# Kernel tuning notes

Measured on AMD Instinct MI355X. Metric: run time of the kernel, lower is better.

Reference implementation:

```python
import jax, jax.numpy as jnp
import numpy as np

BN_EPS = 1e-5


def spmm(rows, cols, vals, x):
    # Sparse [V,V] @ x for x: [B, V, F]. COO (rows, cols, vals) with E nnz.
    B, V, F = x.shape
    xt = jnp.transpose(x, (1, 0, 2)).reshape(V, B * F)      # [V, B*F]
    msg = xt[cols] * vals[:, None]                           # [E, B*F]
    y = jax.ops.segment_sum(msg, rows, num_segments=V)       # [V, B*F]
    return jnp.transpose(y.reshape(V, B, F), (1, 0, 2))      # [B, V, F]


def cheb_conv(rows, cols, vals, x, W, b):
    # Chebyshev graph conv: out = sum_k T_k(L) x @ W[k] + b ; W: [K, Fin, Fout]
    K = W.shape[0]
    x0 = x
    out = jnp.einsum('bvi,io->bvo', x0, W[0])
    if K > 1:
        x1 = spmm(rows, cols, vals, x0)
        out = out + jnp.einsum('bvi,io->bvo', x1, W[1])
        for k in range(2, K):
            x2 = 2.0 * spmm(rows, cols, vals, x1) - x0
            out = out + jnp.einsum('bvi,io->bvo', x2, W[k])
            x0, x1 = x1, x2
    return out + b


def bn_relu(x, gamma, beta):
    # BatchNorm1d (training stats) over (batch, nodes) per channel, then ReLU.
    m = jnp.mean(x, axis=(0, 1))
    v = jnp.var(x, axis=(0, 1))
    y = (x - m) * jax.lax.rsqrt(v + BN_EPS) * gamma + beta
    return jax.nn.relu(y)


def setup_inputs() -> dict:
    key = jax.random.key(0)
    ks = jax.random.split(key, 8)
    V, DEG, B, CIN, COUT = 49152, 20, 2, 128, 64
    x = jax.random.normal(ks[0], (B, V, CIN), dtype=jnp.float32)
    # HEALPix-like sparse Laplacian: diagonal + 20 random neighbors per node
    self_idx = jnp.arange(V, dtype=jnp.int32)
    nbr = jax.random.randint(ks[1], (V * DEG,), 0, V, dtype=jnp.int32)
    rows = jnp.concatenate([self_idx, jnp.repeat(self_idx, DEG)])
    cols = jnp.concatenate([self_idx, nbr])
    vals = jax.random.normal(ks[2], (V * (DEG + 1),), dtype=jnp.float32) * 0.1
    def w(k, shape):
        fan_in = shape[0] * shape[1]
        return jax.random.normal(k, shape, dtype=jnp.float32) * np.float32(np.sqrt(2.0 / fan_in))
    return {
        'x': x, 'rows': rows, 'cols': cols, 'vals': vals,
        'W1': w(ks[3], (1, CIN, COUT)), 'b1': jnp.zeros((COUT,), jnp.float32),
        'g1': jnp.ones((COUT,), jnp.float32), 'be1': jnp.zeros((COUT,), jnp.float32),
        'W2': w(ks[4], (3, COUT, COUT)), 'b2': jnp.zeros((COUT,), jnp.float32),
        'g2': jnp.ones((COUT,), jnp.float32), 'be2': jnp.zeros((COUT,), jnp.float32),
        'W3': w(ks[5], (1, COUT, CIN)), 'b3': jnp.zeros((CIN,), jnp.float32),
        'g3': jnp.ones((CIN,), jnp.float32), 'be3': jnp.zeros((CIN,), jnp.float32),
    }


def reference(x, rows, cols, vals, W1, b1, g1, be1, W2, b2, g2, be2, W3, b3, g3, be3):
    h = bn_relu(cheb_conv(rows, cols, vals, x, W1, b1), g1, be1)   # [B,V,64]
    h = bn_relu(cheb_conv(rows, cols, vals, h, W2, b2), g2, be2)   # [B,V,64]
    h = bn_relu(cheb_conv(rows, cols, vals, h, W3, b3), g3, be3)   # [B,V,128]
    return h
```

## Files before the change

kernel.cpp:

```cpp
#include <hip/hip_runtime.h>

#define VN 49152
#define DEG 20
#define NB 2
#define MROWS (NB * VN)

static constexpr float BN_EPS = 1e-5f;

typedef short bf16x8 __attribute__((ext_vector_type(8)));
typedef float floatx4 __attribute__((ext_vector_type(4)));

__device__ __forceinline__ unsigned short f2bf(float f) {
  unsigned int u = __builtin_bit_cast(unsigned int, f);
  u += 0x7FFFu + ((u >> 16) & 1u);
  return (unsigned short)(u >> 16);
}
__device__ __forceinline__ float bf2f(unsigned short h) {
  unsigned int u = ((unsigned int)h) << 16;
  return __builtin_bit_cast(float, u);
}
__device__ __forceinline__ float bflo(unsigned int u) {
  return __builtin_bit_cast(float, u << 16);
}
__device__ __forceinline__ float bfhi(unsigned int u) {
  return __builtin_bit_cast(float, u & 0xFFFF0000u);
}
__device__ __forceinline__ unsigned int packbf(float a, float b) {
  return (unsigned int)f2bf(a) | ((unsigned int)f2bf(b) << 16);
}
__device__ __forceinline__ void bfunpack8(const uint4& d, float* f) {
  f[0] = bflo(d.x); f[1] = bfhi(d.x); f[2] = bflo(d.y); f[3] = bfhi(d.y);
  f[4] = bflo(d.z); f[5] = bfhi(d.z); f[6] = bflo(d.w); f[7] = bfhi(d.w);
}


#define LDA1 136
__global__ __launch_bounds__(256) void gemm1(const float* __restrict__ X,
    const float* __restrict__ W, const float* __restrict__ bias,
    unsigned short* __restrict__ Y, float* __restrict__ st) {
  __shared__ unsigned short As[128 * LDA1];
  __shared__ unsigned short Bs[64 * LDA1];
  __shared__ float sred[128];
  int t = threadIdx.x;
  int row0 = blockIdx.x * 128;
  if (t < 128) sred[t] = 0.f;
  const float* Xt = X + (size_t)row0 * 128;
  #pragma unroll
  for (int c = 0; c < 16; ++c) {
    int f4i = c * 256 + t;
    int row = f4i >> 5, k = (f4i & 31) * 4;
    float4 v = *(const float4*)(Xt + row * 128 + k);
    *(uint2*)(&As[row * LDA1 + k]) = make_uint2(packbf(v.x, v.y), packbf(v.z, v.w));
  }
  #pragma unroll
  for (int c = 0; c < 32; ++c) {
    int f = c * 256 + t;
    int k = f >> 6, n = f & 63;
    Bs[n * LDA1 + k] = f2bf(W[f]);
  }
  __syncthreads();
  int l = t & 63, wv = t >> 6;
  int lr = l & 15, q = l >> 4;
  int m0 = wv * 32;
  floatx4 acc[2][4];
  #pragma unroll
  for (int mi = 0; mi < 2; ++mi)
    #pragma unroll
    for (int ni = 0; ni < 4; ++ni) acc[mi][ni] = (floatx4)(0.f);
  #pragma unroll
  for (int ks = 0; ks < 128; ks += 32) {
    bf16x8 af[2], bfr[4];
    #pragma unroll
    for (int mi = 0; mi < 2; ++mi)
      af[mi] = *(const bf16x8*)(&As[(m0 + mi * 16 + lr) * LDA1 + ks + q * 8]);
    #pragma unroll
    for (int ni = 0; ni < 4; ++ni)
      bfr[ni] = *(const bf16x8*)(&Bs[(ni * 16 + lr) * LDA1 + ks + q * 8]);
    #pragma unroll
    for (int mi = 0; mi < 2; ++mi)
      #pragma unroll
      for (int ni = 0; ni < 4; ++ni)
        acc[mi][ni] = __builtin_amdgcn_mfma_f32_16x16x32_bf16(af[mi], bfr[ni], acc[mi][ni], 0, 0, 0);
  }
  int b = (row0 >= VN) ? 1 : 0;
  int vbase = row0 - b * VN + m0;
  #pragma unroll
  for (int ni = 0; ni < 4; ++ni) {
    int col = ni * 16 + lr;
    float bv = bias[col];
    size_t sub = (size_t)(b * 2 + (col >> 5)) * VN;
    float s = 0.f, s2 = 0.f;
    #pragma unroll
    for (int mi = 0; mi < 2; ++mi)
      #pragma unroll
      for (int r = 0; r < 4; ++r) {
        float y = acc[mi][ni][r] + bv;
        s += y; s2 += y * y;
        int v = vbase + mi * 16 + q * 4 + r;
        Y[(sub + v) * 32 + (col & 31)] = f2bf(y);
      }
    atomicAdd(&sred[col], s);
    atomicAdd(&sred[64 + col], s2);
  }
  __syncthreads();
  if (t < 128) atomicAdd(&st[t], sred[t]);
}

__global__ __launch_bounds__(256) void spmm1(const unsigned short* __restrict__ T1,
    const int* __restrict__ cols, const float* __restrict__ vals,
    const float* __restrict__ st1, const float* __restrict__ g1,
    const float* __restrict__ be1, unsigned short* __restrict__ X1out) {
  __shared__ float scS[64], shS[64];
  int t = threadIdx.x;
  if (t < 64) {
    float mean = st1[t] * (1.f / MROWS);
    float var = st1[64 + t] * (1.f / MROWS) - mean * mean;
    float sc = g1[t] * rsqrtf(var + BN_EPS);
    scS[t] = sc; shS[t] = be1[t] - mean * sc;
  }
  __syncthreads();
  int g = blockIdx.x;
  int combo = (g & 7) >> 1;
  int rg = ((g >> 3) << 1) | (g & 1);
  int wv = t >> 6, lane = t & 63;
  int v = rg * 64 + wv * 16 + (lane >> 2);
  int ch0 = (lane & 3) * 8;
  int chg = (combo & 1) * 32 + ch0;
  float sc8[8], sh8[8];
  #pragma unroll
  for (int j = 0; j < 8; ++j) { sc8[j] = scS[chg + j]; sh8[j] = shS[chg + j]; }
  const unsigned short* __restrict__ plane = T1 + (size_t)combo * VN * 32;
  int4  c4[5];
  float4 w4[5];
  const int4*   __restrict__ cp4 = (const int4*)(cols + VN + v * DEG);
  const float4* __restrict__ vp4 = (const float4*)(vals + VN + v * DEG);
  #pragma unroll
  for (int j = 0; j < 5; ++j) { c4[j] = cp4[j]; w4[j] = vp4[j]; }
  float a[8];
  {
    float w0 = vals[v];
    uint4 d = *(const uint4*)(plane + (size_t)v * 32 + ch0);
    float f[8]; bfunpack8(d, f);
    #pragma unroll
    for (int j = 0; j < 8; ++j) {
      float h = fmaf(f[j], sc8[j], sh8[j]); h = h > 0.f ? h : 0.f;
      a[j] = w0 * h;
    }
  }
  #pragma unroll
  for (int jj = 0; jj < 5; ++jj) {
    const int cj[4] = {c4[jj].x, c4[jj].y, c4[jj].z, c4[jj].w};
    const float wj[4] = {w4[jj].x, w4[jj].y, w4[jj].z, w4[jj].w};
    #pragma unroll
    for (int e = 0; e < 4; ++e) {
      uint4 d = *(const uint4*)(plane + (size_t)cj[e] * 32 + ch0);
      float f[8]; bfunpack8(d, f);
      float w = wj[e];
      #pragma unroll
      for (int j = 0; j < 8; ++j) {
        float h = fmaf(f[j], sc8[j], sh8[j]); h = h > 0.f ? h : 0.f;
        a[j] = fmaf(h, w, a[j]);
      }
    }
  }
  uint4 o;
  o.x = packbf(a[0], a[1]); o.y = packbf(a[2], a[3]);
  o.z = packbf(a[4], a[5]); o.w = packbf(a[6], a[7]);
  *(uint4*)(X1out + (size_t)combo * VN * 32 + (size_t)v * 32 + ch0) = o;
}

__global__ __launch_bounds__(256) void spmm2(const unsigned short* __restrict__ X1,
    const unsigned short* __restrict__ T1, const int* __restrict__ cols,
    const float* __restrict__ vals, const float* __restrict__ st1,
    const float* __restrict__ g1, const float* __restrict__ be1,
    unsigned short* __restrict__ X2out) {
  __shared__ float scS[64], shS[64];
  int t = threadIdx.x;
  if (t < 64) {
    float mean = st1[t] * (1.f / MROWS);
    float var = st1[64 + t] * (1.f / MROWS) - mean * mean;
    float sc = g1[t] * rsqrtf(var + BN_EPS);
    scS[t] = sc; shS[t] = be1[t] - mean * sc;
  }
  __syncthreads();
  int g = blockIdx.x;
  int combo = (g & 7) >> 1;
  int rg = ((g >> 3) << 1) | (g & 1);
  int wv = t >> 6, lane = t & 63;
  int v = rg * 64 + wv * 16 + (lane >> 2);
  int ch0 = (lane & 3) * 8;
  int chg = (combo & 1) * 32 + ch0;
  const size_t pbase = (size_t)combo * VN * 32;
  const size_t myoff = pbase + (size_t)v * 32 + ch0;
  const unsigned short* __restrict__ plane = X1 + pbase;
  int4  c4[5];
  float4 w4[5];
  const int4*   __restrict__ cp4 = (const int4*)(cols + VN + v * DEG);
  const float4* __restrict__ vp4 = (const float4*)(vals + VN + v * DEG);
  #pragma unroll
  for (int j = 0; j < 5; ++j) { c4[j] = cp4[j]; w4[j] = vp4[j]; }
  float a[8];
  {
    float w0 = vals[v];
    uint4 d = *(const uint4*)(X1 + myoff);
    float f[8]; bfunpack8(d, f);
    #pragma unroll
    for (int j = 0; j < 8; ++j) a[j] = w0 * f[j];
  }
  #pragma unroll
  for (int jj = 0; jj < 5; ++jj) {
    const int cj[4] = {c4[jj].x, c4[jj].y, c4[jj].z, c4[jj].w};
    const float wj[4] = {w4[jj].x, w4[jj].y, w4[jj].z, w4[jj].w};
    #pragma unroll
    for (int e = 0; e < 4; ++e) {
      uint4 d = *(const uint4*)(plane + (size_t)cj[e] * 32 + ch0);
      float f[8]; bfunpack8(d, f);
      float w = wj[e];
      #pragma unroll
      for (int j = 0; j < 8; ++j) a[j] = fmaf(f[j], w, a[j]);
    }
  }
  uint4 tv = *(const uint4*)(T1 + myoff);
  float f[8]; bfunpack8(tv, f);
  float h[8];
  #pragma unroll
  for (int j = 0; j < 8; ++j) {
    float y = fmaf(f[j], scS[chg + j], shS[chg + j]);
    h[j] = y > 0.f ? y : 0.f;
  }
  uint4 o;
  o.x = packbf(2.f * a[0] - h[0], 2.f * a[1] - h[1]);
  o.y = packbf(2.f * a[2] - h[2], 2.f * a[3] - h[3]);
  o.z = packbf(2.f * a[4] - h[4], 2.f * a[5] - h[5]);
  o.w = packbf(2.f * a[6] - h[6], 2.f * a[7] - h[7]);
  *(uint4*)(X2out + myoff) = o;
}

#define LDA2 72
__global__ __launch_bounds__(256) void gemm2(const unsigned short* __restrict__ T1,
    const unsigned short* __restrict__ X1, const unsigned short* __restrict__ X2,
    const float* __restrict__ st1, const float* __restrict__ g1,
    const float* __restrict__ be1, const float* __restrict__ W,
    const float* __restrict__ bias, unsigned short* __restrict__ Y,
    float* __restrict__ st2) {
  __shared__ unsigned short As[128 * LDA2];
  __shared__ unsigned short Bs[64 * LDA2];
  __shared__ float sred[128];
  __shared__ float scS[64], shS[64];
  int t = threadIdx.x;
  int row0 = blockIdx.x * 128;
  int b = (row0 >= VN) ? 1 : 0;
  int b2 = b * 2;
  int vb0 = row0 - b * VN;
  if (t < 128) sred[t] = 0.f;
  if (t < 64) {
    float mean = st1[t] * (1.f / MROWS);
    float var = st1[64 + t] * (1.f / MROWS) - mean * mean;
    float sc = g1[t] * rsqrtf(var + BN_EPS);
    scS[t] = sc; shS[t] = be1[t] - mean * sc;
  }
  __syncthreads();
  int l = t & 63, wv = t >> 6;
  int lr = l & 15, q = l >> 4;
  int m0 = wv * 32;
  floatx4 acc[2][4];
  #pragma unroll
  for (int mi = 0; mi < 2; ++mi)
    #pragma unroll
    for (int ni = 0; ni < 4; ++ni) acc[mi][ni] = (floatx4)(0.f);

  auto stage_b = [&](const float* Wt) {
    #pragma unroll
    for (int c = 0; c < 16; ++c) {
      int f = c * 256 + t;
      int k = f >> 6, n = f & 63;
      Bs[n * LDA2 + k] = f2bf(Wt[f]);
    }
  };
  auto mfma_tile = [&]() {
    #pragma unroll
    for (int ks = 0; ks < 64; ks += 32) {
      bf16x8 af[2], bfr[4];
      #pragma unroll
      for (int mi = 0; mi < 2; ++mi)
        af[mi] = *(const bf16x8*)(&As[(m0 + mi * 16 + lr) * LDA2 + ks + q * 8]);
      #pragma unroll
      for (int ni = 0; ni < 4; ++ni)
        bfr[ni] = *(const bf16x8*)(&Bs[(ni * 16 + lr) * LDA2 + ks + q * 8]);
      #pragma unroll
      for (int mi = 0; mi < 2; ++mi)
        #pragma unroll
        for (int ni = 0; ni < 4; ++ni)
          acc[mi][ni] = __builtin_amdgcn_mfma_f32_16x16x32_bf16(af[mi], bfr[ni], acc[mi][ni], 0, 0, 0);
    }
  };

  #pragma unroll
  for (int c8 = 0; c8 < 8; ++c8) {
    int i = c8 * 256 + t;
    int row = i >> 4, k = (i & 15) * 4;
    const unsigned short* src = T1 + ((size_t)(b2 + (k >> 5)) * VN + vb0 + row) * 32 + (k & 31);
    uint2 rawv = *(const uint2*)src;
    float y0 = fmaf(bflo(rawv.x), scS[k + 0], shS[k + 0]);
    float y1 = fmaf(bfhi(rawv.x), scS[k + 1], shS[k + 1]);
    float y2 = fmaf(bflo(rawv.y), scS[k + 2], shS[k + 2]);
    float y3 = fmaf(bfhi(rawv.y), scS[k + 3], shS[k + 3]);
    y0 = y0 > 0.f ? y0 : 0.f; y1 = y1 > 0.f ? y1 : 0.f;
    y2 = y2 > 0.f ? y2 : 0.f; y3 = y3 > 0.f ? y3 : 0.f;
    *(uint2*)(&As[row * LDA2 + k]) = make_uint2(packbf(y0, y1), packbf(y2, y3));
  }
  stage_b(W);
  __syncthreads();
  mfma_tile();
  __syncthreads();

  #pragma unroll
  for (int c8 = 0; c8 < 8; ++c8) {
    int i = c8 * 256 + t;
    int row = i >> 4, k = (i & 15) * 4;
    const unsigned short* src = X1 + ((size_t)(b2 + (k >> 5)) * VN + vb0 + row) * 32 + (k & 31);
    *(uint2*)(&As[row * LDA2 + k]) = *(const uint2*)src;
  }
  stage_b(W + 64 * 64);
  __syncthreads();
  mfma_tile();
  __syncthreads();

  #pragma unroll
  for (int c8 = 0; c8 < 8; ++c8) {
    int i = c8 * 256 + t;
    int row = i >> 4, k = (i & 15) * 4;
    const unsigned short* src = X2 + ((size_t)(b2 + (k >> 5)) * VN + vb0 + row) * 32 + (k & 31);
    *(uint2*)(&As[row * LDA2 + k]) = *(const uint2*)src;
  }
  stage_b(W + 2 * 64 * 64);
  __syncthreads();
  mfma_tile();

  int vbase = vb0 + m0;
  #pragma unroll
  for (int ni = 0; ni < 4; ++ni) {
    int col = ni * 16 + lr;
    float bv = bias[col];
    size_t sub = (size_t)(b2 + (col >> 5)) * VN;
    float s = 0.f, s2 = 0.f;
    #pragma unroll
    for (int mi = 0; mi < 2; ++mi)
      #pragma unroll
      for (int r = 0; r < 4; ++r) {
        float y = acc[mi][ni][r] + bv;
        s += y; s2 += y * y;
        int v = vbase + mi * 16 + q * 4 + r;
        Y[(sub + v) * 32 + (col & 31)] = f2bf(y);
      }
    atomicAdd(&sred[col], s);
    atomicAdd(&sred[64 + col], s2);
  }
  __syncthreads();
  if (t < 128) atomicAdd(&st2[t], sred[t]);
}

#define LDC3 136
__global__ __launch_bounds__(256) void gemm3(const unsigned short* __restrict__ X,
    const float* __restrict__ W, const float* __restrict__ bias,
    const float* __restrict__ st2, const float* __restrict__ gamma,
    const float* __restrict__ beta, unsigned short* __restrict__ Y,
    float* __restrict__ st3) {
  __shared__ unsigned short smem[18432];
  __shared__ float sred[256];
  __shared__ float scS[64], shS[64];
  unsigned short* As = smem;
  unsigned short* Bs = smem + 128 * LDA2;
  int t = threadIdx.x;
  int row0 = blockIdx.x * 128;
  int b = (row0 >= VN) ? 1 : 0;
  int b2 = b * 2;
  int vb0 = row0 - b * VN;
  sred[t] = 0.f;
  if (t < 64) {
    float mean = st2[t] * (1.f / MROWS);
    float var = st2[64 + t] * (1.f / MROWS) - mean * mean;
    float sc = gamma[t] * rsqrtf(var + BN_EPS);
    scS[t] = sc; shS[t] = beta[t] - mean * sc;
  }
  __syncthreads();
  #pragma unroll
  for (int c8 = 0; c8 < 8; ++c8) {
    int i = c8 * 256 + t;
    int row = i >> 4, k = (i & 15) * 4;
    const unsigned short* src = X + ((size_t)(b2 + (k >> 5)) * VN + vb0 + row) * 32 + (k & 31);
    uint2 rawv = *(const uint2*)src;
    float y0 = fmaf(bflo(rawv.x), scS[k + 0], shS[k + 0]);
    float y1 = fmaf(bfhi(rawv.x), scS[k + 1], shS[k + 1]);
    float y2 = fmaf(bflo(rawv.y), scS[k + 2], shS[k + 2]);
    float y3 = fmaf(bfhi(rawv.y), scS[k + 3], shS[k + 3]);
    y0 = y0 > 0.f ? y0 : 0.f; y1 = y1 > 0.f ? y1 : 0.f;
    y2 = y2 > 0.f ? y2 : 0.f; y3 = y3 > 0.f ? y3 : 0.f;
    *(uint2*)(&As[row * LDA2 + k]) = make_uint2(packbf(y0, y1), packbf(y2, y3));
  }
  #pragma unroll
  for (int c = 0; c < 32; ++c) {
    int f = c * 256 + t;
    int k = f >> 7, n = f & 127;
    Bs[n * LDA2 + k] = f2bf(W[k * 128 + n]);
  }
  __syncthreads();
  int l = t & 63, wv = t >> 6;
  int lr = l & 15, q = l >> 4;
  int m0 = wv * 32;
  floatx4 acc[2][8];
  #pragma unroll
  for (int mi = 0; mi < 2; ++mi)
    #pragma unroll
    for (int ni = 0; ni < 8; ++ni) acc[mi][ni] = (floatx4)(0.f);
  #pragma unroll
  for (int ks = 0; ks < 64; ks += 32) {
    bf16x8 af[2], bfr[8];
    #pragma unroll
    for (int mi = 0; mi < 2; ++mi)
      af[mi] = *(const bf16x8*)(&As[(m0 + mi * 16 + lr) * LDA2 + ks + q * 8]);
    #pragma unroll
    for (int ni = 0; ni < 8; ++ni)
      bfr[ni] = *(const bf16x8*)(&Bs[(ni * 16 + lr) * LDA2 + ks + q * 8]);
    #pragma unroll
    for (int mi = 0; mi < 2; ++mi)
      #pragma unroll
      for (int ni = 0; ni < 8; ++ni)
        acc[mi][ni] = __builtin_amdgcn_mfma_f32_16x16x32_bf16(af[mi], bfr[ni], acc[mi][ni], 0, 0, 0);
  }
  __syncthreads();
  unsigned short* OutS = smem;
  #pragma unroll
  for (int ni = 0; ni < 8; ++ni) {
    int col = ni * 16 + lr;
    float bv = bias[col];
    float s = 0.f, s2 = 0.f;
    #pragma unroll
    for (int mi = 0; mi < 2; ++mi)
      #pragma unroll
      for (int r = 0; r < 4; ++r) {
        float y = acc[mi][ni][r] + bv;
        s += y; s2 += y * y;
        int row = m0 + mi * 16 + q * 4 + r;
        OutS[row * LDC3 + col] = f2bf(y);
      }
    atomicAdd(&sred[col], s);
    atomicAdd(&sred[128 + col], s2);
  }
  __syncthreads();
  atomicAdd(&st3[t], sred[t]);
  #pragma unroll
  for (int c = 0; c < 8; ++c) {
    int idx = c * 256 + t;
    int row = idx >> 4, seg = idx & 15;
    *(uint4*)(Y + ((size_t)(row0 + row)) * 128 + seg * 8) =
        *(const uint4*)(&OutS[row * LDC3 + seg * 8]);
  }
}

__global__ __launch_bounds__(256) void bn_final(const unsigned short* __restrict__ T,
    float* __restrict__ Y, const float* __restrict__ st3,
    const float* __restrict__ gamma, const float* __restrict__ beta) {
  __shared__ float scS[128], shS[128];
  int t = threadIdx.x;
  if (t < 128) {
    float mean = st3[t] * (1.f / MROWS);
    float var = st3[128 + t] * (1.f / MROWS) - mean * mean;
    float sc = gamma[t] * rsqrtf(var + BN_EPS);
    scS[t] = sc;
    shS[t] = beta[t] - mean * sc;
  }
  __syncthreads();
  size_t i4 = ((size_t)blockIdx.x * 256 + t) * 4;
  int c0 = (int)(i4 & 127);
  ushort4 tv = *(const ushort4*)(T + i4);
  unsigned short sv[4] = {tv.x, tv.y, tv.z, tv.w};
  float ov[4];
  #pragma unroll
  for (int j = 0; j < 4; ++j) {
    int c = c0 + j;
    float y = fmaf(bf2f(sv[j]), scS[c], shS[c]);
    ov[j] = y > 0.f ? y : 0.f;
  }
  *(float4*)(Y + i4) = make_float4(ov[0], ov[1], ov[2], ov[3]);
}

extern "C" void kernel_launch(void* const* d_in, const int* in_sizes, int n_in,
                              void* d_out, int out_size, void* d_ws, size_t ws_size,
                              hipStream_t stream) {
  const float* x    = (const float*)d_in[0];
  const int*   cols = (const int*)  d_in[2];
  const float* vals = (const float*)d_in[3];
  const float* W1   = (const float*)d_in[4];
  const float* b1   = (const float*)d_in[5];
  const float* g1   = (const float*)d_in[6];
  const float* be1  = (const float*)d_in[7];
  const float* W2   = (const float*)d_in[8];
  const float* b2   = (const float*)d_in[9];
  const float* g2   = (const float*)d_in[10];
  const float* be2  = (const float*)d_in[11];
  const float* W3   = (const float*)d_in[12];
  const float* b3   = (const float*)d_in[13];
  const float* g3   = (const float*)d_in[14];
  const float* be3  = (const float*)d_in[15];
  float* out = (float*)d_out;

  const size_t PL = (size_t)MROWS * 64;
  unsigned short* P0 = (unsigned short*)d_ws;
  unsigned short* P1 = P0 + PL;
  unsigned short* P2 = P1 + PL;
  unsigned short* P3 = P2 + PL;
  float* st1 = (float*)(P3 + 2 * PL);
  float* st2 = st1 + 128;
  float* st3 = st2 + 128;

  hipMemsetAsync(st1, 0, 512 * sizeof(float), stream);

  dim3 blk(256);
  int rowb = MROWS / 128;
  int spmm_blocks = 3072;
  int ap128_blocks = (int)(PL * 2 / 4 / 256);

  gemm1<<<rowb, blk, 0, stream>>>(x, W1, b1, P0, st1);

  spmm1<<<spmm_blocks, blk, 0, stream>>>(P0, cols, vals, st1, g1, be1, P1);
  spmm2<<<spmm_blocks, blk, 0, stream>>>(P1, P0, cols, vals, st1, g1, be1, P2);
  gemm2<<<rowb, blk, 0, stream>>>(P0, P1, P2, st1, g1, be1, W2, b2, P0, st2);

  gemm3<<<rowb, blk, 0, stream>>>(P0, W3, b3, st2, g2, be2, P3, st3);
  bn_final<<<ap128_blocks, blk, 0, stream>>>(P3, out, st3, g3, be3);
}
```

Baseline: 303.9 us.

## Load GEMM A-operands directly from global into MFMA registers, skipping LDS staging

All three dense GEMM kernels stop staging the activation tile in shared memory and instead load each lane's MFMA A-fragment straight from global memory into registers, fusing the BN+ReLU and bf16 conversion in-register. gemm2 also stages all three Chebyshev weight matrices up front and interleaves the three MFMA terms, removing the intermediate barriers. gemm3 drops the LDS-transposed coalesced output store and writes 2-byte elements directly. The aim is less LDS traffic and fewer syncs. The cost is less coalesced global access, both for the per-lane A loads and for the scattered output stores.

Result: faster. 295.2 us (-2.9%).

```diff
diff --git a/kernel.cpp b/kernel.cpp
--- a/kernel.cpp
+++ b/kernel.cpp
@@ -34,73 +34,72 @@
 }
 
 
-#define LDA1 136
+#define LDB1 136
 __global__ __launch_bounds__(256) void gemm1(const float* __restrict__ X,
     const float* __restrict__ W, const float* __restrict__ bias,
     unsigned short* __restrict__ Y, float* __restrict__ st) {
-  __shared__ unsigned short As[128 * LDA1];
-  __shared__ unsigned short Bs[64 * LDA1];
+  __shared__ unsigned short Bs[64 * LDB1];
   __shared__ float sred[128];
   int t = threadIdx.x;
   int row0 = blockIdx.x * 128;
+  int b = (row0 >= VN) ? 1 : 0;
+  int b2 = b * 2;
+  int vb0 = row0 - b * VN;
   if (t < 128) sred[t] = 0.f;
-  const float* Xt = X + (size_t)row0 * 128;
-  #pragma unroll
-  for (int c = 0; c < 16; ++c) {
-    int f4i = c * 256 + t;
-    int row = f4i >> 5, k = (f4i & 31) * 4;
-    float4 v = *(const float4*)(Xt + row * 128 + k);
-    *(uint2*)(&As[row * LDA1 + k]) = make_uint2(packbf(v.x, v.y), packbf(v.z, v.w));
-  }
   #pragma unroll
   for (int c = 0; c < 32; ++c) {
     int f = c * 256 + t;
     int k = f >> 6, n = f & 63;
-    Bs[n * LDA1 + k] = f2bf(W[f]);
-  }
-  __syncthreads();
-  int l = t & 63, wv = t >> 6;
-  int lr = l & 15, q = l >> 4;
-  int m0 = wv * 32;
-  floatx4 acc[2][4];
-  #pragma unroll
-  for (int mi = 0; mi < 2; ++mi)
-    #pragma unroll
-    for (int ni = 0; ni < 4; ++ni) acc[mi][ni] = (floatx4)(0.f);
-  #pragma unroll
-  for (int ks = 0; ks < 128; ks += 32) {
-    bf16x8 af[2], bfr[4];
-    #pragma unroll
-    for (int mi = 0; mi < 2; ++mi)
-      af[mi] = *(const bf16x8*)(&As[(m0 + mi * 16 + lr) * LDA1 + ks + q * 8]);
-    #pragma unroll
-    for (int ni = 0; ni < 4; ++ni)
-      bfr[ni] = *(const bf16x8*)(&Bs[(ni * 16 + lr) * LDA1 + ks + q * 8]);
-    #pragma unroll
-    for (int mi = 0; mi < 2; ++mi)
-      #pragma unroll
-      for (int ni = 0; ni < 4; ++ni)
-        acc[mi][ni] = __builtin_amdgcn_mfma_f32_16x16x32_bf16(af[mi], bfr[ni], acc[mi][ni], 0, 0, 0);
-  }
-  int b = (row0 >= VN) ? 1 : 0;
-  int vbase = row0 - b * VN + m0;
-  #pragma unroll
-  for (int ni = 0; ni < 4; ++ni) {
-    int col = ni * 16 + lr;
-    float bv = bias[col];
-    size_t sub = (size_t)(b * 2 + (col >> 5)) * VN;
-    float s = 0.f, s2 = 0.f;
-    #pragma unroll
-    for (int mi = 0; mi < 2; ++mi)
+    Bs[n * LDB1 + k] = f2bf(W[f]);
+  }
+  __syncthreads();
+  int lane = t & 63, wv = t >> 6;
+  int lr = lane & 15, q = lane >> 4;
+  float bv4[4];
+  #pragma unroll
+  for (int nt = 0; nt < 4; ++nt) bv4[nt] = bias[nt * 16 + lr];
+  float s4[4] = {0.f, 0.f, 0.f, 0.f}, s24[4] = {0.f, 0.f, 0.f, 0.f};
+  #pragma unroll
+  for (int tile = 0; tile < 2; ++tile) {
+    int vrow = row0 + wv * 32 + tile * 16 + lr;
+    bf16x8 af[4];
+    #pragma unroll
+    for (int kh = 0; kh < 4; ++kh) {
+      const float* xp = X + (size_t)vrow * 128 + kh * 32 + q * 8;
+      float4 a0 = *(const float4*)xp;
+      float4 a1 = *(const float4*)(xp + 4);
+      uint4 u = make_uint4(packbf(a0.x, a0.y), packbf(a0.z, a0.w),
+                           packbf(a1.x, a1.y), packbf(a1.z, a1.w));
+      af[kh] = __builtin_bit_cast(bf16x8, u);
+    }
+    floatx4 acc[4];
+    #pragma unroll
+    for (int nt = 0; nt < 4; ++nt) acc[nt] = (floatx4)(0.f);
+    #pragma unroll
+    for (int kh = 0; kh < 4; ++kh)
+      #pragma unroll
+      for (int nt = 0; nt < 4; ++nt) {
+        bf16x8 bfr = *(const bf16x8*)(&Bs[(nt * 16 + lr) * LDB1 + kh * 32 + q * 8]);
+        acc[nt] = __builtin_amdgcn_mfma_f32_16x16x32_bf16(af[kh], bfr, acc[nt], 0, 0, 0);
+      }
+    int vbase = vb0 + wv * 32 + tile * 16 + q * 4;
+    #pragma unroll
+    for (int nt = 0; nt < 4; ++nt) {
+      int col = nt * 16 + lr;
+      size_t sub = (size_t)(b2 + (col >> 5)) * VN;
       #pragma unroll
       for (int r = 0; r < 4; ++r) {
-        float y = acc[mi][ni][r] + bv;
-        s += y; s2 += y * y;
-        int v = vbase + mi * 16 + q * 4 + r;
-        Y[(sub + v) * 32 + (col & 31)] = f2bf(y);
-      }
-    atomicAdd(&sred[col], s);
-    atomicAdd(&sred[64 + col], s2);
+        float y = acc[nt][r] + bv4[nt];
+        s4[nt] += y; s24[nt] += y * y;
+        Y[(sub + vbase + r) * 32 + (col & 31)] = f2bf(y);
+      }
+    }
+  }
+  #pragma unroll
+  for (int nt = 0; nt < 4; ++nt) {
+    int col = nt * 16 + lr;
+    atomicAdd(&sred[col], s4[nt]);
+    atomicAdd(&sred[64 + col], s24[nt]);
   }
   __syncthreads();
   if (t < 128) atomicAdd(&st[t], sred[t]);
@@ -236,15 +235,14 @@
   *(uint4*)(X2out + myoff) = o;
 }
 
-#define LDA2 72
+#define LDB2 72
 __global__ __launch_bounds__(256) void gemm2(const unsigned short* __restrict__ T1,
     const unsigned short* __restrict__ X1, const unsigned short* __restrict__ X2,
     const float* __restrict__ st1, const float* __restrict__ g1,
     const float* __restrict__ be1, const float* __restrict__ W,
     const float* __restrict__ bias, unsigned short* __restrict__ Y,
     float* __restrict__ st2) {
-  __shared__ unsigned short As[128 * LDA2];
-  __shared__ unsigned short Bs[64 * LDA2];
+  __shared__ unsigned short Bs[3 * 64 * LDB2];
   __shared__ float sred[128];
   __shared__ float scS[64], shS[64];
   int t = threadIdx.x;
@@ -259,118 +257,94 @@
     float sc = g1[t] * rsqrtf(var + BN_EPS);
     scS[t] = sc; shS[t] = be1[t] - mean * sc;
   }
-  __syncthreads();
-  int l = t & 63, wv = t >> 6;
-  int lr = l & 15, q = l >> 4;
-  int m0 = wv * 32;
-  floatx4 acc[2][4];
-  #pragma unroll
-  for (int mi = 0; mi < 2; ++mi)
-    #pragma unroll
-    for (int ni = 0; ni < 4; ++ni) acc[mi][ni] = (floatx4)(0.f);
-
-  auto stage_b = [&](const float* Wt) {
-    #pragma unroll
-    for (int c = 0; c < 16; ++c) {
-      int f = c * 256 + t;
-      int k = f >> 6, n = f & 63;
-      Bs[n * LDA2 + k] = f2bf(Wt[f]);
-    }
-  };
-  auto mfma_tile = [&]() {
-    #pragma unroll
-    for (int ks = 0; ks < 64; ks += 32) {
-      bf16x8 af[2], bfr[4];
-      #pragma unroll
-      for (int mi = 0; mi < 2; ++mi)
-        af[mi] = *(const bf16x8*)(&As[(m0 + mi * 16 + lr) * LDA2 + ks + q * 8]);
-      #pragma unroll
-      for (int ni = 0; ni < 4; ++ni)
-        bfr[ni] = *(const bf16x8*)(&Bs[(ni * 16 + lr) * LDA2 + ks + q * 8]);
-      #pragma unroll
-      for (int mi = 0; mi < 2; ++mi)
-        #pragma unroll
-        for (int ni = 0; ni < 4; ++ni)
-          acc[mi][ni] = __builtin_amdgcn_mfma_f32_16x16x32_bf16(af[mi], bfr[ni], acc[mi][ni], 0, 0, 0);
-    }
-  };
-
-  #pragma unroll
-  for (int c8 = 0; c8 < 8; ++c8) {
-    int i = c8 * 256 + t;
-    int row = i >> 4, k = (i & 15) * 4;
-    const unsigned short* src = T1 + ((size_t)(b2 + (k >> 5)) * VN + vb0 + row) * 32 + (k & 31);
-    uint2 rawv = *(const uint2*)src;
-    float y0 = fmaf(bflo(rawv.x), scS[k + 0], shS[k + 0]);
-    float y1 = fmaf(bfhi(rawv.x), scS[k + 1], shS[k + 1]);
-    float y2 = fmaf(bflo(rawv.y), scS[k + 2], shS[k + 2]);
-    float y3 = fmaf(bfhi(rawv.y), scS[k + 3], shS[k + 3]);
-    y0 = y0 > 0.f ? y0 : 0.f; y1 = y1 > 0.f ? y1 : 0.f;
-    y2 = y2 > 0.f ? y2 : 0.f; y3 = y3 > 0.f ? y3 : 0.f;
-    *(uint2*)(&As[row * LDA2 + k]) = make_uint2(packbf(y0, y1), packbf(y2, y3));
-  }
-  stage_b(W);
-  __syncthreads();
-  mfma_tile();
-  __syncthreads();
-
-  #pragma unroll
-  for (int c8 = 0; c8 < 8; ++c8) {
-    int i = c8 * 256 + t;
-    int row = i >> 4, k = (i & 15) * 4;
-    const unsigned short* src = X1 + ((size_t)(b2 + (k >> 5)) * VN + vb0 + row) * 32 + (k & 31);
-    *(uint2*)(&As[row * LDA2 + k]) = *(const uint2*)src;
-  }
-  stage_b(W + 64 * 64);
-  __syncthreads();
-  mfma_tile();
-  __syncthreads();
-
-  #pragma unroll
-  for (int c8 = 0; c8 < 8; ++c8) {
-    int i = c8 * 256 + t;
-    int row = i >> 4, k = (i & 15) * 4;
-    const unsigned short* src = X2 + ((size_t)(b2 + (k >> 5)) * VN + vb0 + row) * 32 + (k & 31);
-    *(uint2*)(&As[row * LDA2 + k]) = *(const uint2*)src;
-  }
-  stage_b(W + 2 * 64 * 64);
-  __syncthreads();
-  mfma_tile();
-
-  int vbase = vb0 + m0;
-  #pragma unroll
-  for (int ni = 0; ni < 4; ++ni) {
-    int col = ni * 16 + lr;
-    float bv = bias[col];
-    size_t sub = (size_t)(b2 + (col >> 5)) * VN;
-    float s = 0.f, s2 = 0.f;
-    #pragma unroll
-    for (int mi = 0; mi < 2; ++mi)
+  #pragma unroll
+  for (int c = 0; c < 48; ++c) {
+    int f = c * 256 + t;
+    int term = f >> 12, rem = f & 4095;
+    int k = rem >> 6, n = rem & 63;
+    Bs[term * 64 * LDB2 + n * LDB2 + k] = f2bf(W[f]);
+  }
+  __syncthreads();
+  int lane = t & 63, wv = t >> 6;
+  int lr = lane & 15, q = lane >> 4;
+  float bv4[4];
+  #pragma unroll
+  for (int nt = 0; nt < 4; ++nt) bv4[nt] = bias[nt * 16 + lr];
+  float sc8[8], sh8[8];
+  #pragma unroll
+  for (int kh = 0; kh < 2; ++kh)
+    #pragma unroll
+    for (int j = 0; j < 4; ++j) {
+      sc8[kh * 4 + j] = scS[kh * 32 + q * 8 + j + 0];
+      sh8[kh * 4 + j] = shS[kh * 32 + q * 8 + j + 0];
+    }
+  float s4[4] = {0.f, 0.f, 0.f, 0.f}, s24[4] = {0.f, 0.f, 0.f, 0.f};
+  #pragma unroll
+  for (int tile = 0; tile < 2; ++tile) {
+    int vrow = vb0 + wv * 32 + tile * 16 + lr;
+    bf16x8 af0[2], af1[2], af2[2];
+    #pragma unroll
+    for (int kh = 0; kh < 2; ++kh) {
+      size_t off = ((size_t)(b2 + kh) * VN + vrow) * 32 + q * 8;
+      uint4 d0 = *(const uint4*)(T1 + off);
+      float f8[8]; bfunpack8(d0, f8);
+      #pragma unroll
+      for (int j = 0; j < 8; ++j) {
+        float y = fmaf(f8[j], scS[kh * 32 + q * 8 + j], shS[kh * 32 + q * 8 + j]);
+        f8[j] = y > 0.f ? y : 0.f;
+      }
+      uint4 u = make_uint4(packbf(f8[0], f8[1]), packbf(f8[2], f8[3]),
+                           packbf(f8[4], f8[5]), packbf(f8[6], f8[7]));
+      af0[kh] = __builtin_bit_cast(bf16x8, u);
+      af1[kh] = __builtin_bit_cast(bf16x8, *(const uint4*)(X1 + off));
+      af2[kh] = __builtin_bit_cast(bf16x8, *(const uint4*)(X2 + off));
+    }
+    floatx4 acc[4];
+    #pragma unroll
+    for (int nt = 0; nt < 4; ++nt) acc[nt] = (floatx4)(0.f);
+    #pragma unroll
+    for (int kh = 0; kh < 2; ++kh)
+      #pragma unroll
+      for (int nt = 0; nt < 4; ++nt) {
+        int bo = (nt * 16 + lr) * LDB2 + kh * 32 + q * 8;
+        acc[nt] = __builtin_amdgcn_mfma_f32_16x16x32_bf16(
+            af0[kh], *(const bf16x8*)(&Bs[bo]), acc[nt], 0, 0, 0);
+        acc[nt] = __builtin_amdgcn_mfma_f32_16x16x32_bf16(
+            af1[kh], *(const bf16x8*)(&Bs[64 * LDB2 + bo]), acc[nt], 0, 0, 0);
+        acc[nt] = __builtin_amdgcn_mfma_f32_16x16x32_bf16(
+            af2[kh], *(const bf16x8*)(&Bs[2 * 64 * LDB2 + bo]), acc[nt], 0, 0, 0);
+      }
+    int vbase = vb0 + wv * 32 + tile * 16 + q * 4;
+    #pragma unroll
+    for (int nt = 0; nt < 4; ++nt) {
+      int col = nt * 16 + lr;
+      size_t sub = (size_t)(b2 + (col >> 5)) * VN;
       #pragma unroll
       for (int r = 0; r < 4; ++r) {
-        float y = acc[mi][ni][r] + bv;
-        s += y; s2 += y * y;
-        int v = vbase + mi * 16 + q * 4 + r;
-        Y[(sub + v) * 32 + (col & 31)] = f2bf(y);
-      }
-    atomicAdd(&sred[col], s);
-    atomicAdd(&sred[64 + col], s2);
+        float y = acc[nt][r] + bv4[nt];
+        s4[nt] += y; s24[nt] += y * y;
+        Y[(sub + vbase + r) * 32 + (col & 31)] = f2bf(y);
+      }
+    }
+  }
+  #pragma unroll
+  for (int nt = 0; nt < 4; ++nt) {
+    int col = nt * 16 + lr;
+    atomicAdd(&sred[col], s4[nt]);
+    atomicAdd(&sred[64 + col], s24[nt]);
   }
   __syncthreads();
   if (t < 128) atomicAdd(&st2[t], sred[t]);
 }
 
-#define LDC3 136
-__global__ __launch_bounds__(256) void gemm3(const unsigned short* __restrict__ X,
+__global__ __launch_bounds__(256) void gemm3(const unsigned short* __restrict__ T2,
     const float* __restrict__ W, const float* __restrict__ bias,
-    const float* __restrict__ st2, const float* __restrict__ gamma,
-    const float* __restrict__ beta, unsigned short* __restrict__ Y,
+    const float* __restrict__ st2, const float* __restrict__ g2,
+    const float* __restrict__ be2, unsigned short* __restrict__ Y,
     float* __restrict__ st3) {
-  __shared__ unsigned short smem[18432];
+  __shared__ unsigned short Bs[128 * LDB2];
   __shared__ float sred[256];
   __shared__ float scS[64], shS[64];
-  unsigned short* As = smem;
-  unsigned short* Bs = smem + 128 * LDA2;
   int t = threadIdx.x;
   int row0 = blockIdx.x * 128;
   int b = (row0 >= VN) ? 1 : 0;
@@ -380,82 +354,70 @@
   if (t < 64) {
     float mean = st2[t] * (1.f / MROWS);
     float var = st2[64 + t] * (1.f / MROWS) - mean * mean;
-    float sc = gamma[t] * rsqrtf(var + BN_EPS);
-    scS[t] = sc; shS[t] = beta[t] - mean * sc;
-  }
-  __syncthreads();
-  #pragma unroll
-  for (int c8 = 0; c8 < 8; ++c8) {
-    int i = c8 * 256 + t;
-    int row = i >> 4, k = (i & 15) * 4;
-    const unsigned short* src = X + ((size_t)(b2 + (k >> 5)) * VN + vb0 + row) * 32 + (k & 31);
-    uint2 rawv = *(const uint2*)src;
-    float y0 = fmaf(bflo(rawv.x), scS[k + 0], shS[k + 0]);
-    float y1 = fmaf(bfhi(rawv.x), scS[k + 1], shS[k + 1]);
-    float y2 = fmaf(bflo(rawv.y), scS[k + 2], shS[k + 2]);
-    float y3 = fmaf(bfhi(rawv.y), scS[k + 3], shS[k + 3]);
-    y0 = y0 > 0.f ? y0 : 0.f; y1 = y1 > 0.f ? y1 : 0.f;
-    y2 = y2 > 0.f ? y2 : 0.f; y3 = y3 > 0.f ? y3 : 0.f;
-    *(uint2*)(&As[row * LDA2 + k]) = make_uint2(packbf(y0, y1), packbf(y2, y3));
+    float sc = g2[t] * rsqrtf(var + BN_EPS);
+    scS[t] = sc; shS[t] = be2[t] - mean * sc;
   }
   #pragma unroll
   for (int c = 0; c < 32; ++c) {
     int f = c * 256 + t;
     int k = f >> 7, n = f & 127;
-    Bs[n * LDA2 + k] = f2bf(W[k * 128 + n]);
-  }
-  __syncthreads();
-  int l = t & 63, wv = t >> 6;
-  int lr = l & 15, q = l >> 4;
-  int m0 = wv * 32;
-  floatx4 acc[2][8];
-  #pragma unroll
-  for (int mi = 0; mi < 2; ++mi)
-    #pragma unroll
-    for (int ni = 0; ni < 8; ++ni) acc[mi][ni] = (floatx4)(0.f);
-  #pragma unroll
-  for (int ks = 0; ks < 64; ks += 32) {
-    bf16x8 af[2], bfr[8];
-    #pragma unroll
-    for (int mi = 0; mi < 2; ++mi)
-      af[mi] = *(const bf16x8*)(&As[(m0 + mi * 16 + lr) * LDA2 + ks + q * 8]);
-    #pragma unroll
-    for (int ni = 0; ni < 8; ++ni)
-      bfr[ni] = *(const bf16x8*)(&Bs[(ni * 16 + lr) * LDA2 + ks + q * 8]);
-    #pragma unroll
-    for (int mi = 0; mi < 2; ++mi)
-      #pragma unroll
-      for (int ni = 0; ni < 8; ++ni)
-        acc[mi][ni] = __builtin_amdgcn_mfma_f32_16x16x32_bf16(af[mi], bfr[ni], acc[mi][ni], 0, 0, 0);
-  }
-  __syncthreads();
-  unsigned short* OutS = smem;
-  #pragma unroll
-  for (int ni = 0; ni < 8; ++ni) {
-    int col = ni * 16 + lr;
-    float bv = bias[col];
-    float s = 0.f, s2 = 0.f;
-    #pragma unroll
-    for (int mi = 0; mi < 2; ++mi)
+    Bs[n * LDB2 + k] = f2bf(W[k * 128 + n]);
+  }
+  __syncthreads();
+  int lane = t & 63, wv = t >> 6;
+  int lr = lane & 15, q = lane >> 4;
+  float bv8[8];
+  #pragma unroll
+  for (int nt = 0; nt < 8; ++nt) bv8[nt] = bias[nt * 16 + lr];
+  float s8[8] = {0.f,0.f,0.f,0.f,0.f,0.f,0.f,0.f};
+  float s28[8] = {0.f,0.f,0.f,0.f,0.f,0.f,0.f,0.f};
+  #pragma unroll
+  for (int tile = 0; tile < 2; ++tile) {
+    int vrow = vb0 + wv * 32 + tile * 16 + lr;
+    bf16x8 af[2];
+    #pragma unroll
+    for (int kh = 0; kh < 2; ++kh) {
+      uint4 d = *(const uint4*)(T2 + ((size_t)(b2 + kh) * VN + vrow) * 32 + q * 8);
+      float f8[8]; bfunpack8(d, f8);
+      #pragma unroll
+      for (int j = 0; j < 8; ++j) {
+        float y = fmaf(f8[j], scS[kh * 32 + q * 8 + j], shS[kh * 32 + q * 8 + j]);
+        f8[j] = y > 0.f ? y : 0.f;
+      }
+      uint4 u = make_uint4(packbf(f8[0], f8[1]), packbf(f8[2], f8[3]),
+                           packbf(f8[4], f8[5]), packbf(f8[6], f8[7]));
+      af[kh] = __builtin_bit_cast(bf16x8, u);
+    }
+    floatx4 acc[8];
+    #pragma unroll
+    for (int nt = 0; nt < 8; ++nt) acc[nt] = (floatx4)(0.f);
+    #pragma unroll
+    for (int kh = 0; kh < 2; ++kh)
+      #pragma unroll
+      for (int nt = 0; nt < 8; ++nt) {
+        bf16x8 bfr = *(const bf16x8*)(&Bs[(nt * 16 + lr) * LDB2 + kh * 32 + q * 8]);
+        acc[nt] = __builtin_amdgcn_mfma_f32_16x16x32_bf16(af[kh], bfr, acc[nt], 0, 0, 0);
+      }
+    int rbase = row0 + wv * 32 + tile * 16 + q * 4;
+    #pragma unroll
+    for (int nt = 0; nt < 8; ++nt) {
+      int col = nt * 16 + lr;
       #pragma unroll
       for (int r = 0; r < 4; ++r) {
-        float y = acc[mi][ni][r] + bv;
-        s += y; s2 += y * y;
-        int row = m0 + mi * 16 + q * 4 + r;
-        OutS[row * LDC3 + col] = f2bf(y);
-      }
-    atomicAdd(&sred[col], s);
-    atomicAdd(&sred[128 + col], s2);
+        float y = acc[nt][r] + bv8[nt];
+        s8[nt] += y; s28[nt] += y * y;
+        Y[(size_t)(rbase + r) * 128 + col] = f2bf(y);
+      }
+    }
+  }
+  #pragma unroll
+  for (int nt = 0; nt < 8; ++nt) {
+    int col = nt * 16 + lr;
+    atomicAdd(&sred[col], s8[nt]);
+    atomicAdd(&sred[128 + col], s28[nt]);
   }
   __syncthreads();
   atomicAdd(&st3[t], sred[t]);
-  #pragma unroll
-  for (int c = 0; c < 8; ++c) {
-    int idx = c * 256 + t;
-    int row = idx >> 4, seg = idx & 15;
-    *(uint4*)(Y + ((size_t)(row0 + row)) * 128 + seg * 8) =
-        *(const uint4*)(&OutS[row * LDC3 + seg * 8]);
-  }
 }
 
 __global__ __launch_bounds__(256) void bn_final(const unsigned short* __restrict__ T,
```
